# Performance work log

Measured on AMD Instinct MI355X. Metric: run time of the kernel, lower is better.

The kernel has to match this reference:

```python
import jax, jax.numpy as jnp
import numpy as np

DIM = 384
HEADS = 8
SR = 2
EPS = 1e-5


def setup_inputs() -> dict:
    key = jax.random.key(0)
    ks = jax.random.split(key, 10)
    B, H, W, C = 16, 56, 56, DIM
    s = 0.02
    return {
        "x": jax.random.normal(ks[0], (B, H * W, C), jnp.float32),
        "qkv_w": jax.random.normal(ks[1], (3 * C, C), jnp.float32) * s,
        "qkv_b": jnp.zeros((3 * C,), jnp.float32),
        "proj_w": jax.random.normal(ks[2], (C, C), jnp.float32) * s,
        "proj_b": jnp.zeros((C,), jnp.float32),
        "lp_w": jax.random.normal(ks[3], (C, SR, SR), jnp.float32) * s,  # depthwise convT weight (C,1,sr,sr) squeezed
        "lp_b": jnp.zeros((C,), jnp.float32),
        "ln_w": jnp.ones((C,), jnp.float32),
        "ln_b": jnp.zeros((C,), jnp.float32),
        "H": 56,
        "W": 56,
    }


def reference(x, qkv_w, qkv_b, proj_w, proj_b, lp_w, lp_b, ln_w, ln_b, H, W):
    B, N, C = x.shape
    hd = C // HEADS
    scale = hd ** -0.5

    # AvgPool2d(kernel=(1,1), stride=(sr,sr)) == strided subsampling
    xi = x.transpose(0, 2, 1).reshape(B, C, H, W)[:, :, ::SR, ::SR]
    h, w = H // SR, W // SR
    n = h * w
    xs = xi.reshape(B, C, n).transpose(0, 2, 1)  # [B, n, C]

    qkv = (xs @ qkv_w.T + qkv_b).reshape(B, n, 3, HEADS, hd).transpose(2, 0, 3, 1, 4)
    q, k, v = qkv[0], qkv[1], qkv[2]  # each [B, heads, n, hd]

    attn = jax.nn.softmax(jnp.einsum('bhqd,bhkd->bhqk', q, k) * scale, axis=-1)
    o = jnp.einsum('bhqk,bhkd->bhqd', attn, v).transpose(0, 2, 1, 3).reshape(B, n, C)

    # ConvTranspose2d(C, C, kernel=sr, stride=sr, groups=C): each input pixel
    # expands to an sr x sr block scaled by the per-channel kernel.
    oi = o.transpose(0, 2, 1).reshape(B, C, h, w)
    up = jnp.einsum('bchw,cpq->bchpwq', oi, lp_w).reshape(B, C, H, W)
    up = up + lp_b[None, :, None, None]

    y = up.reshape(B, C, N).transpose(0, 2, 1)  # [B, N, C]
    mu = y.mean(-1, keepdims=True)
    var = y.var(-1, keepdims=True)
    y = (y - mu) * jax.lax.rsqrt(var + EPS) * ln_w + ln_b

    return y @ proj_w.T + proj_b
```

## Files before the change

### kernel.cpp

```cpp
#include <hip/hip_runtime.h>
#include <math.h>

#define CDIM 384
#define NHEADS 8
#define HD 48
#define NQ 784
#define NQPAD 832
#define NB 16
#define HWD 56
#define NPIX 3136
#define QK_SCALE (0.14433756729740643f * 1.4426950408889634f)
#define LN_EPS 1e-5f
#define WSCALE 16.0f
#define WUNSCALE 0.0625f

typedef _Float16 f16;
typedef _Float16 f16x4 __attribute__((ext_vector_type(4)));
typedef _Float16 f16x8 __attribute__((ext_vector_type(8)));
typedef float f32x4 __attribute__((ext_vector_type(4)));

__device__ __forceinline__ float waveSum(float v) {
#pragma unroll
  for (int o = 32; o > 0; o >>= 1) v += __shfl_xor(v, o);
  return v;
}

__device__ __forceinline__ float fast_exp2(float x) {
#if __has_builtin(__builtin_amdgcn_exp2f)
  return __builtin_amdgcn_exp2f(x);
#else
  return __expf(x * 0.6931471805599453f);
#endif
}

__device__ __forceinline__ void gload16(const void* g, void* l) {
  __builtin_amdgcn_global_load_lds(
      (const __attribute__((address_space(1))) void*)g,
      (__attribute__((address_space(3))) void*)l, 16, 0, 0);
}

__global__ __launch_bounds__(256) void zero_kernel(float4* __restrict__ p,
                                                   int n4) {
  const int i = blockIdx.x * 256 + threadIdx.x;
  if (i < n4) p[i] = make_float4(0.f, 0.f, 0.f, 0.f);
}

__global__ __launch_bounds__(256) void pool_cast_kernel(
    const float* __restrict__ x, f16* __restrict__ xp) {
  const int i = (blockIdx.x * 256 + threadIdx.x) * 4;
  const int row = i / CDIM, col = i % CDIM;
  const int b = row / NQ, qi = row % NQ;
  const int hi = qi / 28, wi = qi % 28;
  const float4 v =
      *(const float4*)(x + ((size_t)(b * NPIX + hi * 112 + wi * 2)) * CDIM + col);
  f16x4 h;
  h.x = (f16)v.x; h.y = (f16)v.y; h.z = (f16)v.z; h.w = (f16)v.w;
  *(f16x4*)(xp + i) = h;
}

__global__ __launch_bounds__(256) void w_cast_kernel(
    const float* __restrict__ src, f16* __restrict__ dst, int n) {
  const int i = (blockIdx.x * 256 + threadIdx.x) * 4;
  if (i >= n) return;
  const float4 v = *(const float4*)(src + i);
  f16x4 h;
  h.x = (f16)v.x; h.y = (f16)v.y; h.z = (f16)v.z; h.w = (f16)v.w;
  *(f16x4*)(dst + i) = h;
}

__device__ __forceinline__ void mfma_tile_gemm(
    const f16* __restrict__ A, const f16* __restrict__ B, int m0, int n0,
    int K, f32x4 (&acc)[4][4], f16* As, f16* Bs) {
  const int t = threadIdx.x;
  const int lane = t & 63, w = t >> 6;
  const int wm = w >> 1, wn = w & 1;
  const int l15 = lane & 15, l4 = lane >> 4;

  const int rowS = t >> 2;
  const int kb = (t & 3) * 16;
  char* AsB = (char*)As;
  char* BsB = (char*)Bs;
  const char* Ag = (const char*)A;
  const char* Bg = (const char*)B;

  for (int k0 = 0; k0 < K; k0 += 32) {
    gload16(Ag + (((size_t)(m0 + rowS) * K + k0) * 2 + kb), AsB + t * 16);
    gload16(Ag + (((size_t)(m0 + rowS + 64) * K + k0) * 2 + kb),
            AsB + 4096 + t * 16);
    gload16(Bg + (((size_t)(n0 + rowS) * K + k0) * 2 + kb), BsB + t * 16);
    gload16(Bg + (((size_t)(n0 + rowS + 64) * K + k0) * 2 + kb),
            BsB + 4096 + t * 16);
    __syncthreads();
    f16x8 af[4], bf[4];
#pragma unroll
    for (int i = 0; i < 4; ++i)
      af[i] = *(const f16x8*)(AsB + ((wm * 64 + i * 16 + l15) * 64 + l4 * 16));
#pragma unroll
    for (int j = 0; j < 4; ++j)
      bf[j] = *(const f16x8*)(BsB + ((wn * 64 + j * 16 + l15) * 64 + l4 * 16));
#pragma unroll
    for (int i = 0; i < 4; ++i)
#pragma unroll
      for (int j = 0; j < 4; ++j)
        acc[i][j] =
            __builtin_amdgcn_mfma_f32_16x16x32_f16(af[i], bf[j], acc[i][j], 0, 0, 0);
    __syncthreads();
  }
}

__global__ __launch_bounds__(256) void qkv_mfma_kernel(
    const f16* __restrict__ xp, const f16* __restrict__ wh,
    const float* __restrict__ qkv_b, f16* __restrict__ qh,
    f16* __restrict__ kh, f16* __restrict__ vt) {
  __shared__ f16 As[128 * 32];
  __shared__ f16 Bs[128 * 32];
  const int m0 = blockIdx.x * 128, n0 = blockIdx.y * 128;
  f32x4 acc[4][4] = {};
  mfma_tile_gemm(xp, wh, m0, n0, CDIM, acc, As, Bs);

  const int t = threadIdx.x, lane = t & 63, w = t >> 6;
  const int wm = w >> 1, wn = w & 1;
  const int l15 = lane & 15, l4 = lane >> 4;
#pragma unroll
  for (int j = 0; j < 4; ++j) {
    const int f = n0 + wn * 64 + j * 16 + l15;
    const int sec = f / CDIM, fr = f % CDIM;
    const int hh = fr / HD, d = fr % HD;
    const float bias = qkv_b[f];
#pragma unroll
    for (int i = 0; i < 4; ++i) {
#pragma unroll
      for (int r = 0; r < 4; ++r) {
        const int mm = m0 + wm * 64 + i * 16 + l4 * 4 + r;
        const int bb = mm / NQ, qi = mm % NQ;
        const int bh = bb * NHEADS + hh;
        const float val = acc[i][j][r] + bias;
        if (sec == 0)
          qh[((size_t)bh * NQ + qi) * 64 + d] = (f16)(val * QK_SCALE);
        else if (sec == 1)
          kh[((size_t)bh * NQ + qi) * 64 + d] = (f16)val;
        else
          vt[((size_t)bh * HD + d) * NQPAD + qi] = (f16)val;
      }
    }
  }
}

__global__ __launch_bounds__(256) void flash_kernel(
    const f16* __restrict__ qh, const f16* __restrict__ kh,
    const f16* __restrict__ vt, f16* __restrict__ o16) {
  __shared__ f16 PQ[128 * 72];
  __shared__ f16 Ks[64][72];
  __shared__ f16 Vts[48][72];

  f16 (*Qs)[72] = (f16(*)[72])PQ;
  f16 (*Ps)[32][68] = (f16(*)[32][68])PQ;

  const int t = threadIdx.x;
  const int lane = t & 63, w = t >> 6;
  const int quad = lane >> 4, l15 = lane & 15;
  const int q0 = blockIdx.x * 128;
  const int bh = blockIdx.y;

  const f16* qg = qh + (size_t)bh * NQ * 64;
  const f16* kg = kh + (size_t)bh * NQ * 64;
  const f16* vg = vt + (size_t)bh * HD * NQPAD;

  {
    const f16x8 z8 = {};
    *(f16x8*)&Qs[t >> 1][48 + (t & 1) * 8] = z8;
    if (t < 128) *(f16x8*)&Ks[t >> 1][48 + (t & 1) * 8] = z8;
  }

#pragma unroll
  for (int c = 0; c < 3; ++c) {
    const int u = t + c * 256;
    const int row = u / 6, seg = u % 6;
    const int gr = min(q0 + row, NQ - 1);
    *(f16x8*)&Qs[row][seg * 8] =
        *(const f16x8*)(qg + (size_t)gr * 64 + seg * 8);
  }
  __syncthreads();

  f16x8 qf0[2], qf1[2];
#pragma unroll
  for (int qa = 0; qa < 2; ++qa) {
    const int row = w * 32 + qa * 16 + l15;
    qf0[qa] = *(const f16x8*)&Qs[row][quad * 8];
    qf1[qa] = *(const f16x8*)&Qs[row][32 + quad * 8];
  }

  const f16* gp[3];
  f16* lp[3];
  int step[3];
#pragma unroll
  for (int c = 0; c < 3; ++c) {
    const int u = t + c * 256;
    if (u < 384) {
      const int row = u / 6, seg = u % 6;
      gp[c] = kg + (size_t)row * 64 + seg * 8;
      lp[c] = &Ks[row][seg * 8];
      step[c] = 64 * 64;
    } else {
      const int uv = u - 384;
      const int row = uv >> 3, seg = uv & 7;
      gp[c] = vg + (size_t)row * NQPAD + seg * 8;
      lp[c] = &Vts[row][seg * 8];
      step[c] = 64;
    }
  }

  f16x8 rg[3];
#pragma unroll
  for (int c = 0; c < 3; ++c) {
    rg[c] = *(const f16x8*)gp[c];
    gp[c] += step[c];
  }

  f32x4 accO[2][3] = {};
  float l_[2][4] = {};

  for (int kt = 0; kt < 13; ++kt) {
#pragma unroll
    for (int c = 0; c < 3; ++c) *(f16x8*)lp[c] = rg[c];
    __syncthreads();
    if (kt < 12) {
#pragma unroll
      for (int c = 0; c < 3; ++c) {
        rg[c] = *(const f16x8*)gp[c];
        gp[c] += step[c];
      }
    }

    const bool last = (kt == 12);
#pragma unroll
    for (int j = 0; j < 4; ++j) {
      const f16x8 b0 = *(const f16x8*)&Ks[j * 16 + l15][quad * 8];
      const f16x8 b1 = *(const f16x8*)&Ks[j * 16 + l15][32 + quad * 8];
      f32x4 z0 = {}, z1 = {};
      z0 = __builtin_amdgcn_mfma_f32_16x16x32_f16(qf0[0], b0, z0, 0, 0, 0);
      const f32x4 sj0 = __builtin_amdgcn_mfma_f32_16x16x32_f16(qf1[0], b1, z0, 0, 0, 0);
      z1 = __builtin_amdgcn_mfma_f32_16x16x32_f16(qf0[1], b0, z1, 0, 0, 0);
      const f32x4 sj1 = __builtin_amdgcn_mfma_f32_16x16x32_f16(qf1[1], b1, z1, 0, 0, 0);
      const bool msk = last && (j >= 1);
#pragma unroll
      for (int r = 0; r < 4; ++r) {
        const float p0 = msk ? 0.f : fast_exp2(sj0[r]);
        const float p1 = msk ? 0.f : fast_exp2(sj1[r]);
        l_[0][r] += p0;
        l_[1][r] += p1;
        Ps[w][quad * 4 + r][j * 16 + l15] = (f16)p0;
        Ps[w][16 + quad * 4 + r][j * 16 + l15] = (f16)p1;
      }
    }

    f16x8 ap0[2], ap1[2];
#pragma unroll
    for (int qa = 0; qa < 2; ++qa) {
      const int row = qa * 16 + l15;
      const f16x4 a0 = *(const f16x4*)&Ps[w][row][quad * 8];
      const f16x4 a1 = *(const f16x4*)&Ps[w][row][quad * 8 + 4];
      const f16x4 a2 = *(const f16x4*)&Ps[w][row][32 + quad * 8];
      const f16x4 a3 = *(const f16x4*)&Ps[w][row][32 + quad * 8 + 4];
      ap0[qa] = __builtin_shufflevector(a0, a1, 0, 1, 2, 3, 4, 5, 6, 7);
      ap1[qa] = __builtin_shufflevector(a2, a3, 0, 1, 2, 3, 4, 5, 6, 7);
    }

#pragma unroll
    for (int jn = 0; jn < 3; ++jn) {
      const f16x8 v0 = *(const f16x8*)&Vts[jn * 16 + l15][quad * 8];
      const f16x8 v1 = *(const f16x8*)&Vts[jn * 16 + l15][32 + quad * 8];
#pragma unroll
      for (int qa = 0; qa < 2; ++qa) {
        accO[qa][jn] =
            __builtin_amdgcn_mfma_f32_16x16x32_f16(ap0[qa], v0, accO[qa][jn], 0, 0, 0);
        accO[qa][jn] =
            __builtin_amdgcn_mfma_f32_16x16x32_f16(ap1[qa], v1, accO[qa][jn], 0, 0, 0);
      }
    }
    __syncthreads();
  }

  const int b = bh >> 3, hh = bh & 7;
#pragma unroll
  for (int qa = 0; qa < 2; ++qa) {
#pragma unroll
    for (int r = 0; r < 4; ++r) {
      float rs = l_[qa][r];
      rs += __shfl_xor(rs, 1);
      rs += __shfl_xor(rs, 2);
      rs += __shfl_xor(rs, 4);
      rs += __shfl_xor(rs, 8);
      const int qrow = q0 + w * 32 + qa * 16 + quad * 4 + r;
      if (qrow < NQ) {
        const float inv = 1.f / rs;
#pragma unroll
        for (int jn = 0; jn < 3; ++jn)
          o16[((size_t)(b * NQ + qrow)) * CDIM + hh * HD + jn * 16 + l15] =
              (f16)(accO[qa][jn][r] * inv);
      }
    }
  }
}

__global__ __launch_bounds__(256) void stats_kernel(
    const f16* __restrict__ o16, const float* __restrict__ lp_w,
    const float* __restrict__ lp_b, float* __restrict__ stats) {
  const int m = blockIdx.x * 4 + (threadIdx.x >> 6);
  const int lane = threadIdx.x & 63;
  float s[4] = {}, ss[4] = {};
#pragma unroll
  for (int i = 0; i < 6; ++i) {
    const int c = lane + i * 64;
    const float ov = (float)o16[(size_t)m * CDIM + c];
    const float4 w4 = *(const float4*)(lp_w + c * 4);
    const float bb = lp_b[c];
    const float u0 = ov * w4.x + bb;
    const float u1 = ov * w4.y + bb;
    const float u2 = ov * w4.z + bb;
    const float u3 = ov * w4.w + bb;
    s[0] += u0; ss[0] += u0 * u0;
    s[1] += u1; ss[1] += u1 * u1;
    s[2] += u2; ss[2] += u2 * u2;
    s[3] += u3; ss[3] += u3 * u3;
  }
#pragma unroll
  for (int pq = 0; pq < 4; ++pq) {
    s[pq] = waveSum(s[pq]);
    ss[pq] = waveSum(ss[pq]);
  }
  if (lane < 4) {
    const float mu = s[lane] * (1.f / CDIM);
    const float var = ss[lane] * (1.f / CDIM) - mu * mu;
    stats[m * 8 + lane * 2] = mu;
    stats[m * 8 + lane * 2 + 1] = rsqrtf(var + LN_EPS);
  }
}

__global__ __launch_bounds__(256) void wprep_kernel(
    const float* __restrict__ pw, const float* __restrict__ lpw,
    const float* __restrict__ lnw, f16* __restrict__ wq) {
  const int i4 = (blockIdx.x * 256 + threadIdx.x) * 4;
  const int f = i4 / CDIM, c = i4 % CDIM;
  const int pq = f / CDIM, j = f % CDIM;
  const float4 wv = *(const float4*)(pw + (size_t)j * CDIM + c);
  const float4 ln = *(const float4*)(lnw + c);
  f16x4 h;
  h.x = (f16)(wv.x * lpw[(c + 0) * 4 + pq] * ln.x * WSCALE);
  h.y = (f16)(wv.y * lpw[(c + 1) * 4 + pq] * ln.y * WSCALE);
  h.z = (f16)(wv.z * lpw[(c + 2) * 4 + pq] * ln.z * WSCALE);
  h.w = (f16)(wv.w * lpw[(c + 3) * 4 + pq] * ln.w * WSCALE);
  *(f16x4*)(wq + i4) = h;
}

__global__ __launch_bounds__(64) void cvec_kernel(
    const float* __restrict__ pw, const float* __restrict__ lp_b,
    const float* __restrict__ ln_w, const float* __restrict__ ln_b,
    const float* __restrict__ pb, float* __restrict__ cvec) {
  const int j = blockIdx.x;
  const int lane = threadIdx.x;
  float a1 = 0.f, a2 = 0.f, a3 = 0.f;
#pragma unroll
  for (int i = 0; i < 6; ++i) {
    const int c = lane + i * 64;
    const float wv = pw[(size_t)j * CDIM + c];
    a1 += lp_b[c] * ln_w[c] * wv;
    a2 += ln_w[c] * wv;
    a3 += ln_b[c] * wv;
  }
  a1 = waveSum(a1);
  a2 = waveSum(a2);
  a3 = waveSum(a3);
  if (lane == 0) {
    cvec[j] = a1;
    cvec[CDIM + j] = a2;
    cvec[2 * CDIM + j] = a3 + pb[j];
  }
}

__global__ __launch_bounds__(256) void projfused_kernel(
    const f16* __restrict__ o16, const f16* __restrict__ wq,
    const float* __restrict__ stats, const float* __restrict__ cvec,
    float* __restrict__ out) {
  __shared__ f16 As[128 * 32];
  __shared__ f16 Bs[128 * 32];
  const int m0 = blockIdx.x * 128, n0 = blockIdx.y * 128;
  f32x4 acc[4][4] = {};
  mfma_tile_gemm(o16, wq, m0, n0, CDIM, acc, As, Bs);

  const int t = threadIdx.x, lane = t & 63, w = t >> 6;
  const int wm = w >> 1, wn = w & 1;
  const int l15 = lane & 15, l4 = lane >> 4;
  const int pq = n0 / CDIM;
  const int p = pq >> 1, q = pq & 1;
  const int c0 = n0 - pq * CDIM;

  float C1[4], C2[4], C3[4];
#pragma unroll
  for (int j = 0; j < 4; ++j) {
    const int col = c0 + wn * 64 + j * 16 + l15;
    C1[j] = cvec[col];
    C2[j] = cvec[CDIM + col];
    C3[j] = cvec[2 * CDIM + col];
  }

#pragma unroll
  for (int i = 0; i < 4; ++i) {
#pragma unroll
    for (int r = 0; r < 4; ++r) {
      const int m = m0 + wm * 64 + i * 16 + l4 * 4 + r;
      const int b = m / NQ, n = m % NQ;
      const int hi2 = n / 28, wi2 = n % 28;
      const float mu = stats[m * 8 + pq * 2];
      const float rstd = stats[m * 8 + pq * 2 + 1];
      const int pix = (hi2 * 2 + p) * HWD + (wi2 * 2 + q);
      float* orow = out + ((size_t)(b * NPIX + pix)) * CDIM;
#pragma unroll
      for (int j = 0; j < 4; ++j) {
        const int col = c0 + wn * 64 + j * 16 + l15;
        orow[col] = rstd * (acc[i][j][r] * WUNSCALE + C1[j] - mu * C2[j]) + C3[j];
      }
    }
  }
}

extern "C" void kernel_launch(void* const* d_in, const int* in_sizes, int n_in,
                              void* d_out, int out_size, void* d_ws,
                              size_t ws_size, hipStream_t stream) {
  const float* x      = (const float*)d_in[0];
  const float* qkv_w  = (const float*)d_in[1];
  const float* qkv_b  = (const float*)d_in[2];
  const float* proj_w = (const float*)d_in[3];
  const float* proj_b = (const float*)d_in[4];
  const float* lp_w   = (const float*)d_in[5];
  const float* lp_b   = (const float*)d_in[6];
  const float* ln_w   = (const float*)d_in[7];
  const float* ln_b   = (const float*)d_in[8];
  float* out = (float*)d_out;

  float* ws = (float*)d_ws;
  f16* o16 = (f16*)ws;
  float* zreg = ws + 2408448;
  f16* qh = (f16*)zreg;
  f16* kh = qh + (size_t)128 * NQ * 64;
  f16* vt = kh + (size_t)128 * NQ * 64;
  float* rest = zreg + 8978432;
  f16* xp = (f16*)rest;
  f16* qkv_wh = xp + (size_t)12544 * CDIM;
  float* rest2 = rest + 2408448 + 221184;
  f16* wq = (f16*)rest2;
  float* cvec = rest2 + 1179648;
  float* stats = cvec + 1152;

  zero_kernel<<<dim3(2496), 256, 0, stream>>>((float4*)(zreg + 6422528), 638976);

  pool_cast_kernel<<<dim3(4704), 256, 0, stream>>>(x, xp);
  w_cast_kernel<<<dim3(432), 256, 0, stream>>>(qkv_w, qkv_wh, 1152 * CDIM);
  qkv_mfma_kernel<<<dim3(98, 9), 256, 0, stream>>>(xp, qkv_wh, qkv_b, qh, kh, vt);

  flash_kernel<<<dim3(7, 128), 256, 0, stream>>>(qh, kh, vt, o16);

  stats_kernel<<<dim3(3136), 256, 0, stream>>>(o16, lp_w, lp_b, stats);
  wprep_kernel<<<dim3(576), 256, 0, stream>>>(proj_w, lp_w, ln_w, wq);
  cvec_kernel<<<dim3(384), 64, 0, stream>>>(proj_w, lp_b, ln_w, ln_b, proj_b,
                                            cvec);

  projfused_kernel<<<dim3(98, 12), 256, 0, stream>>>(o16, wq, stats, cvec, out);
}
```

Measured before the change: 281.2 us.

## Double-buffer LDS in MFMA GEMM tiles and remap blocks per XCD

The shared GEMM tile routine now double-buffers its LDS stages, issuing the next K-slice's global-to-LDS loads before computing on the current one, and drops one barrier per iteration. The QKV and projection kernels switch to a 1D grid whose block index is remapped so that consecutive tiles land on the same XCD, which should improve L2 reuse of the shared A/B rows. LDS use per block doubles, which may reduce occupancy, and the single barrier per iteration relies on the loads into the other buffer not racing with reads still in flight.

New measurement: 275.2 us. 1.02x faster.

```diff
diff --git a/kernel.cpp b/kernel.cpp
--- a/kernel.cpp
+++ b/kernel.cpp
@@ -39,6 +39,13 @@
       (__attribute__((address_space(3))) void*)l, 16, 0, 0);
 }
 
+__device__ __forceinline__ int xcd_chunk_lin(int b, int nwg) {
+  const int c = b & 7, s = b >> 3;
+  const int q = nwg >> 3, r = nwg & 7;
+  const int off = (c < r) ? c * (q + 1) : r * (q + 1) + (c - r) * q;
+  return off + s;
+}
+
 __global__ __launch_bounds__(256) void zero_kernel(float4* __restrict__ p,
                                                    int n4) {
   const int i = blockIdx.x * 256 + threadIdx.x;
@@ -68,43 +75,54 @@
   *(f16x4*)(dst + i) = h;
 }
 
-__device__ __forceinline__ void mfma_tile_gemm(
+__device__ __forceinline__ void mfma_tile_gemm_db(
     const f16* __restrict__ A, const f16* __restrict__ B, int m0, int n0,
     int K, f32x4 (&acc)[4][4], f16* As, f16* Bs) {
   const int t = threadIdx.x;
   const int lane = t & 63, w = t >> 6;
   const int wm = w >> 1, wn = w & 1;
   const int l15 = lane & 15, l4 = lane >> 4;
-
   const int rowS = t >> 2;
   const int kb = (t & 3) * 16;
   char* AsB = (char*)As;
   char* BsB = (char*)Bs;
-  const char* Ag = (const char*)A;
-  const char* Bg = (const char*)B;
-
+  const char* Ag = (const char*)A + ((size_t)(m0 + rowS) * K) * 2 + kb;
+  const char* Bg = (const char*)B + ((size_t)(n0 + rowS) * K) * 2 + kb;
+  const size_t row64 = (size_t)64 * K * 2;
+
+  gload16(Ag, AsB + t * 16);
+  gload16(Ag + row64, AsB + 4096 + t * 16);
+  gload16(Bg, BsB + t * 16);
+  gload16(Bg + row64, BsB + 4096 + t * 16);
+
+  int cur = 0;
   for (int k0 = 0; k0 < K; k0 += 32) {
-    gload16(Ag + (((size_t)(m0 + rowS) * K + k0) * 2 + kb), AsB + t * 16);
-    gload16(Ag + (((size_t)(m0 + rowS + 64) * K + k0) * 2 + kb),
-            AsB + 4096 + t * 16);
-    gload16(Bg + (((size_t)(n0 + rowS) * K + k0) * 2 + kb), BsB + t * 16);
-    gload16(Bg + (((size_t)(n0 + rowS + 64) * K + k0) * 2 + kb),
-            BsB + 4096 + t * 16);
     __syncthreads();
+    if (k0 + 32 < K) {
+      const int nb_ = cur ^ 1;
+      const char* Ag2 = Ag + (size_t)(k0 + 32) * 2;
+      const char* Bg2 = Bg + (size_t)(k0 + 32) * 2;
+      gload16(Ag2, AsB + nb_ * 8192 + t * 16);
+      gload16(Ag2 + row64, AsB + nb_ * 8192 + 4096 + t * 16);
+      gload16(Bg2, BsB + nb_ * 8192 + t * 16);
+      gload16(Bg2 + row64, BsB + nb_ * 8192 + 4096 + t * 16);
+    }
+    const char* Ab = AsB + cur * 8192;
+    const char* Bb = BsB + cur * 8192;
     f16x8 af[4], bf[4];
 #pragma unroll
     for (int i = 0; i < 4; ++i)
-      af[i] = *(const f16x8*)(AsB + ((wm * 64 + i * 16 + l15) * 64 + l4 * 16));
+      af[i] = *(const f16x8*)(Ab + ((wm * 64 + i * 16 + l15) * 64 + l4 * 16));
 #pragma unroll
     for (int j = 0; j < 4; ++j)
-      bf[j] = *(const f16x8*)(BsB + ((wn * 64 + j * 16 + l15) * 64 + l4 * 16));
+      bf[j] = *(const f16x8*)(Bb + ((wn * 64 + j * 16 + l15) * 64 + l4 * 16));
 #pragma unroll
     for (int i = 0; i < 4; ++i)
 #pragma unroll
       for (int j = 0; j < 4; ++j)
         acc[i][j] =
             __builtin_amdgcn_mfma_f32_16x16x32_f16(af[i], bf[j], acc[i][j], 0, 0, 0);
-    __syncthreads();
+    cur ^= 1;
   }
 }
 
@@ -112,11 +130,12 @@
     const f16* __restrict__ xp, const f16* __restrict__ wh,
     const float* __restrict__ qkv_b, f16* __restrict__ qh,
     f16* __restrict__ kh, f16* __restrict__ vt) {
-  __shared__ f16 As[128 * 32];
-  __shared__ f16 Bs[128 * 32];
-  const int m0 = blockIdx.x * 128, n0 = blockIdx.y * 128;
+  __shared__ f16 As[2 * 128 * 32];
+  __shared__ f16 Bs[2 * 128 * 32];
+  const int lin = xcd_chunk_lin(blockIdx.x, 882);
+  const int m0 = (lin / 9) * 128, n0 = (lin % 9) * 128;
   f32x4 acc[4][4] = {};
-  mfma_tile_gemm(xp, wh, m0, n0, CDIM, acc, As, Bs);
+  mfma_tile_gemm_db(xp, wh, m0, n0, CDIM, acc, As, Bs);
 
   const int t = threadIdx.x, lane = t & 63, w = t >> 6;
   const int wm = w >> 1, wn = w & 1;
@@ -382,11 +401,12 @@
     const f16* __restrict__ o16, const f16* __restrict__ wq,
     const float* __restrict__ stats, const float* __restrict__ cvec,
     float* __restrict__ out) {
-  __shared__ f16 As[128 * 32];
-  __shared__ f16 Bs[128 * 32];
-  const int m0 = blockIdx.x * 128, n0 = blockIdx.y * 128;
+  __shared__ f16 As[2 * 128 * 32];
+  __shared__ f16 Bs[2 * 128 * 32];
+  const int lin = xcd_chunk_lin(blockIdx.x, 1176);
+  const int m0 = (lin / 12) * 128, n0 = (lin % 12) * 128;
   f32x4 acc[4][4] = {};
-  mfma_tile_gemm(o16, wq, m0, n0, CDIM, acc, As, Bs);
+  mfma_tile_gemm_db(o16, wq, m0, n0, CDIM, acc, As, Bs);
 
   const int t = threadIdx.x, lane = t & 63, w = t >> 6;
   const int wm = w >> 1, wn = w & 1;
@@ -456,7 +476,7 @@
 
   pool_cast_kernel<<<dim3(4704), 256, 0, stream>>>(x, xp);
   w_cast_kernel<<<dim3(432), 256, 0, stream>>>(qkv_w, qkv_wh, 1152 * CDIM);
-  qkv_mfma_kernel<<<dim3(98, 9), 256, 0, stream>>>(xp, qkv_wh, qkv_b, qh, kh, vt);
+  qkv_mfma_kernel<<<dim3(882), 256, 0, stream>>>(xp, qkv_wh, qkv_b, qh, kh, vt);
 
   flash_kernel<<<dim3(7, 128), 256, 0, stream>>>(qh, kh, vt, o16);
 
@@ -465,5 +485,5 @@
   cvec_kernel<<<dim3(384), 64, 0, stream>>>(proj_w, lp_b, ln_w, ln_b, proj_b,
                                             cvec);
 
-  projfused_kernel<<<dim3(98, 12), 256, 0, stream>>>(o16, wq, stats, cvec, out);
-}
+  projfused_kernel<<<dim3(1176), 256, 0, stream>>>(o16, wq, stats, cvec, out);
+}
```

## Load full-K tiles into swizzled LDS and remap blocks per XCD for GEMMs

Applied to the files above, without the earlier changes.

Both the QKV and projection GEMMs now stage the entire K=384 slab of a 64x128 tile into LDS in one shot with an XOR swizzle, then run the MFMA loop with no per-step barriers. The M tile shrinks from 128 to 64, doubling the block count, and a 1D grid is remapped so consecutive tiles land on the same XCD for L2 reuse. The aim is to cut synchronisation and bank conflicts and improve cache locality. In exchange each block uses about 144KB of LDS, which limits occupancy to one block per CU, and global loads are no longer overlapped with compute.

Result: slower. 288.6 us (+2.6%).

```diff
diff --git a/kernel.cpp b/kernel.cpp
--- a/kernel.cpp
+++ b/kernel.cpp
@@ -39,6 +39,13 @@
       (__attribute__((address_space(3))) void*)l, 16, 0, 0);
 }
 
+__device__ __forceinline__ int xcd_chunk_lin(int b, int nwg) {
+  const int c = b & 7, s = b >> 3;
+  const int q = nwg >> 3, r = nwg & 7;
+  const int off = (c < r) ? c * (q + 1) : r * (q + 1) + (c - r) * q;
+  return off + s;
+}
+
 __global__ __launch_bounds__(256) void zero_kernel(float4* __restrict__ p,
                                                    int n4) {
   const int i = blockIdx.x * 256 + threadIdx.x;
@@ -68,43 +75,56 @@
   *(f16x4*)(dst + i) = h;
 }
 
-__device__ __forceinline__ void mfma_tile_gemm(
+__device__ __forceinline__ void mfma_fullk_gemm(
     const f16* __restrict__ A, const f16* __restrict__ B, int m0, int n0,
-    int K, f32x4 (&acc)[4][4], f16* As, f16* Bs) {
+    f32x4 (&acc)[2][4], f16* As , f16* Bs ) {
   const int t = threadIdx.x;
   const int lane = t & 63, w = t >> 6;
   const int wm = w >> 1, wn = w & 1;
   const int l15 = lane & 15, l4 = lane >> 4;
-
-  const int rowS = t >> 2;
-  const int kb = (t & 3) * 16;
+  const char* Ag = (const char*)A;
+  const char* Bg = (const char*)B;
   char* AsB = (char*)As;
   char* BsB = (char*)Bs;
-  const char* Ag = (const char*)A;
-  const char* Bg = (const char*)B;
-
-  for (int k0 = 0; k0 < K; k0 += 32) {
-    gload16(Ag + (((size_t)(m0 + rowS) * K + k0) * 2 + kb), AsB + t * 16);
-    gload16(Ag + (((size_t)(m0 + rowS + 64) * K + k0) * 2 + kb),
-            AsB + 4096 + t * 16);
-    gload16(Bg + (((size_t)(n0 + rowS) * K + k0) * 2 + kb), BsB + t * 16);
-    gload16(Bg + (((size_t)(n0 + rowS + 64) * K + k0) * 2 + kb),
-            BsB + 4096 + t * 16);
-    __syncthreads();
-    f16x8 af[4], bf[4];
-#pragma unroll
-    for (int i = 0; i < 4; ++i)
-      af[i] = *(const f16x8*)(AsB + ((wm * 64 + i * 16 + l15) * 64 + l4 * 16));
-#pragma unroll
-    for (int j = 0; j < 4; ++j)
-      bf[j] = *(const f16x8*)(BsB + ((wn * 64 + j * 16 + l15) * 64 + l4 * 16));
-#pragma unroll
-    for (int i = 0; i < 4; ++i)
+
+#pragma unroll
+  for (int c = 0; c < 36; ++c) {
+    const int u = t + c * 256;
+    if (c < 12) {
+      const int row = u / 48, seg = u % 48;
+      gload16(Ag + (((size_t)(m0 + row) * 384 + (seg ^ (row & 7)) * 8) * 2),
+              AsB + u * 16);
+    } else {
+      const int v = u - 3072;
+      const int row = v / 48, seg = v % 48;
+      gload16(Bg + (((size_t)(n0 + row) * 384 + (seg ^ (row & 7)) * 8) * 2),
+              BsB + v * 16);
+    }
+  }
+  __syncthreads();
+
+#pragma unroll
+  for (int ks = 0; ks < 12; ++ks) {
+    const int c0 = ks * 4;
+    f16x8 af[2], bf[4];
+#pragma unroll
+    for (int i = 0; i < 2; ++i) {
+      const int row = wm * 32 + i * 16 + l15;
+      const int ch = (c0 + l4) ^ (row & 7);
+      af[i] = *(const f16x8*)(AsB + row * 768 + ch * 16);
+    }
+#pragma unroll
+    for (int j = 0; j < 4; ++j) {
+      const int row = wn * 64 + j * 16 + l15;
+      const int ch = (c0 + l4) ^ (row & 7);
+      bf[j] = *(const f16x8*)(BsB + row * 768 + ch * 16);
+    }
+#pragma unroll
+    for (int i = 0; i < 2; ++i)
 #pragma unroll
       for (int j = 0; j < 4; ++j)
         acc[i][j] =
             __builtin_amdgcn_mfma_f32_16x16x32_f16(af[i], bf[j], acc[i][j], 0, 0, 0);
-    __syncthreads();
   }
 }
 
@@ -112,11 +132,12 @@
     const f16* __restrict__ xp, const f16* __restrict__ wh,
     const float* __restrict__ qkv_b, f16* __restrict__ qh,
     f16* __restrict__ kh, f16* __restrict__ vt) {
-  __shared__ f16 As[128 * 32];
-  __shared__ f16 Bs[128 * 32];
-  const int m0 = blockIdx.x * 128, n0 = blockIdx.y * 128;
-  f32x4 acc[4][4] = {};
-  mfma_tile_gemm(xp, wh, m0, n0, CDIM, acc, As, Bs);
+  __shared__ f16 As[64 * 384];
+  __shared__ f16 Bs[128 * 384];
+  const int lin = xcd_chunk_lin(blockIdx.x, 1764);
+  const int m0 = (lin / 9) * 64, n0 = (lin % 9) * 128;
+  f32x4 acc[2][4] = {};
+  mfma_fullk_gemm(xp, wh, m0, n0, acc, As, Bs);
 
   const int t = threadIdx.x, lane = t & 63, w = t >> 6;
   const int wm = w >> 1, wn = w & 1;
@@ -128,10 +149,10 @@
     const int hh = fr / HD, d = fr % HD;
     const float bias = qkv_b[f];
 #pragma unroll
-    for (int i = 0; i < 4; ++i) {
+    for (int i = 0; i < 2; ++i) {
 #pragma unroll
       for (int r = 0; r < 4; ++r) {
-        const int mm = m0 + wm * 64 + i * 16 + l4 * 4 + r;
+        const int mm = m0 + wm * 32 + i * 16 + l4 * 4 + r;
         const int bb = mm / NQ, qi = mm % NQ;
         const int bh = bb * NHEADS + hh;
         const float val = acc[i][j][r] + bias;
@@ -382,11 +403,12 @@
     const f16* __restrict__ o16, const f16* __restrict__ wq,
     const float* __restrict__ stats, const float* __restrict__ cvec,
     float* __restrict__ out) {
-  __shared__ f16 As[128 * 32];
-  __shared__ f16 Bs[128 * 32];
-  const int m0 = blockIdx.x * 128, n0 = blockIdx.y * 128;
-  f32x4 acc[4][4] = {};
-  mfma_tile_gemm(o16, wq, m0, n0, CDIM, acc, As, Bs);
+  __shared__ f16 As[64 * 384];
+  __shared__ f16 Bs[128 * 384];
+  const int lin = xcd_chunk_lin(blockIdx.x, 2352);
+  const int m0 = (lin / 12) * 64, n0 = (lin % 12) * 128;
+  f32x4 acc[2][4] = {};
+  mfma_fullk_gemm(o16, wq, m0, n0, acc, As, Bs);
 
   const int t = threadIdx.x, lane = t & 63, w = t >> 6;
   const int wm = w >> 1, wn = w & 1;
@@ -405,10 +427,10 @@
   }
 
 #pragma unroll
-  for (int i = 0; i < 4; ++i) {
+  for (int i = 0; i < 2; ++i) {
 #pragma unroll
     for (int r = 0; r < 4; ++r) {
-      const int m = m0 + wm * 64 + i * 16 + l4 * 4 + r;
+      const int m = m0 + wm * 32 + i * 16 + l4 * 4 + r;
       const int b = m / NQ, n = m % NQ;
       const int hi2 = n / 28, wi2 = n % 28;
       const float mu = stats[m * 8 + pq * 2];
@@ -456,7 +478,7 @@
 
   pool_cast_kernel<<<dim3(4704), 256, 0, stream>>>(x, xp);
   w_cast_kernel<<<dim3(432), 256, 0, stream>>>(qkv_w, qkv_wh, 1152 * CDIM);
-  qkv_mfma_kernel<<<dim3(98, 9), 256, 0, stream>>>(xp, qkv_wh, qkv_b, qh, kh, vt);
+  qkv_mfma_kernel<<<dim3(1764), 256, 0, stream>>>(xp, qkv_wh, qkv_b, qh, kh, vt);
 
   flash_kernel<<<dim3(7, 128), 256, 0, stream>>>(qh, kh, vt, o16);
 
@@ -465,5 +487,5 @@
   cvec_kernel<<<dim3(384), 64, 0, stream>>>(proj_w, lp_b, ln_w, ln_b, proj_b,
                                             cvec);
 
-  projfused_kernel<<<dim3(98, 12), 256, 0, stream>>>(o16, wq, stats, cvec, out);
-}
+  projfused_kernel<<<dim3(2352), 256, 0, stream>>>(o16, wq, stats, cvec, out);
+}
```
